# Performance work log

Hardware: AMD Instinct MI355X
Metric: run time of the kernel (lower is better)

The kernel has to match this reference:

```python
import jax, jax.numpy as jnp
import numpy as np

H = 1024      # hidden_size
NH = 16       # num_heads
HD = 128      # head_dim
ID = NH * HD  # inner_dim = 2048
EPS = 1e-6


def setup_inputs() -> dict:
    key = jax.random.key(0)
    ks = jax.random.split(key, 8)
    n = lambda k, shape, sc=1.0: jax.random.normal(k, shape, dtype=jnp.float32) * sc
    return {
        "x": n(ks[0], (1, H)),
        "rnn_state": n(ks[1], (1, NH, HD, HD)),
        "conv_state": n(ks[2], (1, 3 * ID, 3)),
        # learned parameters (nn.Linear stores W as [out_features, in_features])
        "W_qkv": n(ks[3], (3 * ID, H), 0.02),
        "W_z": n(ks[4], (ID, H), 0.02),
        "W_a": n(ks[5], (NH, H), 0.02),
        "norm_w": jnp.ones((HD,), jnp.float32),
        "W_out": n(ks[6], (H, ID), 0.02),
    }


def reference(x, rnn_state, conv_state, W_qkv, W_z, W_a, norm_w, W_out):
    # QKV projection: [1, 3*ID]
    qkv = x @ W_qkv.T
    q, k, v = jnp.split(qkv, 3, axis=-1)
    q = q.reshape(-1, NH, HD)
    k = k.reshape(-1, NH, HD)
    v = v.reshape(-1, NH, HD)

    # per-head scalar decay in (0,1): [1, NH, 1, 1]
    decay = jax.nn.sigmoid(x @ W_a.T)[:, :, None, None]

    # outer product k \otimes v: [1, NH, HD, HD]
    kv = k[..., :, None] * v[..., None, :]
    new_state = rnn_state * decay + kv

    # query readout: [1, NH, HD]
    y = jnp.einsum('bhd,bhde->bhe', q, new_state)

    # RMSNorm over head_dim
    y = y * jax.lax.rsqrt(jnp.mean(y * y, axis=-1, keepdims=True) + EPS) * norm_w
    y = y.reshape(-1, ID)

    # silu-gated combine and output projection
    z = x @ W_z.T
    y = y * (z * jax.nn.sigmoid(z))
    out = y @ W_out.T
    return (out, new_state, conv_state)
```

## Files before the change

### kernel.cpp

```cpp
#include <hip/hip_runtime.h>
#include <math.h>

#define H    1024
#define NH   16
#define HD   128
#define ID   2048
#define NROWS_A (3*ID + ID + NH)
#define MATVEC_BLOCKS (NROWS_A / 4)
#define CONV_FLOATS (3 * ID * 3)
#define CONV_BLOCKS (CONV_FLOATS / 4 / 256)
#define EPS 1e-6f

__device__ __forceinline__ float waveReduceSum(float v) {
#pragma unroll
    for (int off = 32; off > 0; off >>= 1) v += __shfl_down(v, off, 64);
    return v;
}
__device__ __forceinline__ float waveReduceSumAll(float v) {
#pragma unroll
    for (int off = 1; off < 64; off <<= 1) v += __shfl_xor(v, off, 64);
    return v;
}

__global__ __launch_bounds__(256) void matvec_qkvza(
    const float* __restrict__ x,
    const float* __restrict__ Wqkv,
    const float* __restrict__ Wz,
    const float* __restrict__ Wa,
    const float* __restrict__ conv,
    float* __restrict__ conv_out,
    float* __restrict__ out,
    float* __restrict__ ws_qkv,
    float* __restrict__ ws_zsig,
    float* __restrict__ ws_decay)
{
    if (blockIdx.x >= MATVEC_BLOCKS) {
        const int cb = blockIdx.x - MATVEC_BLOCKS;
        const int i = cb * 256 + threadIdx.x;
        ((float4*)conv_out)[i] = ((const float4*)conv)[i];
        if (cb == 0) {
            float4 z4 = {0.f, 0.f, 0.f, 0.f};
            ((float4*)out)[threadIdx.x] = z4;
        }
        return;
    }

    const int wave = threadIdx.x >> 6;
    const int lane = threadIdx.x & 63;
    const int r = blockIdx.x * 4 + wave;

    const float* row;
    if (r < 3 * ID)           row = Wqkv + (size_t)r * H;
    else if (r < 3 * ID + ID) row = Wz   + (size_t)(r - 3 * ID) * H;
    else                      row = Wa   + (size_t)(r - 3 * ID - ID) * H;

    const float4* row4 = (const float4*)row;
    const float4* x4   = (const float4*)x;

    float acc = 0.f;
#pragma unroll
    for (int t = 0; t < 4; ++t) {
        float4 w  = row4[lane + 64 * t];
        float4 xv = x4[lane + 64 * t];
        acc += w.x * xv.x + w.y * xv.y + w.z * xv.z + w.w * xv.w;
    }
    acc = waveReduceSum(acc);
    if (lane == 0) {
        if (r < 3 * ID) {
            ws_qkv[r] = acc;
        } else if (r < 3 * ID + ID) {
            const float sig = 1.f / (1.f + expf(-acc));
            ws_zsig[r - 3 * ID] = acc * sig;
        } else {
            ws_decay[r - 3 * ID - ID] = 1.f / (1.f + expf(-acc));
        }
    }
}

__global__ __launch_bounds__(1024) void state_gate_out(
    const float* __restrict__ state_in,
    const float* __restrict__ ws_qkv,
    const float* __restrict__ ws_decay,
    const float* __restrict__ ws_zsig,
    const float* __restrict__ normw,
    const float* __restrict__ Wout,
    float* __restrict__ state_out,
    float* __restrict__ out)
{
    const int h  = blockIdx.x >> 4;
    const int s  = blockIdx.x & 15;
    const int t  = threadIdx.x;
    const int c  = t & 31;
    const int dg = t >> 5;
    const int wv = t >> 6;
    const int lane = t & 63;

    __shared__ float4 part4[16][32];
    __shared__ float gated[HD];
    __shared__ float red2[2];

    const float decay = ws_decay[h];
    const float4 vv = ((const float4*)(ws_qkv + 2 * ID + h * HD))[c];
    const float4 q4 = ((const float4*)(ws_qkv + h * HD))[dg];
    const float4 k4 = ((const float4*)(ws_qkv + ID + h * HD))[dg];

    const float4* sin4 = (const float4*)(state_in  + (size_t)h * HD * HD);
    float4*       sout = (float4*)(state_out + (size_t)h * HD * HD);

    const bool do_write = (wv == s);

    float4 acc = {0.f, 0.f, 0.f, 0.f};
    const float qs[4] = {q4.x, q4.y, q4.z, q4.w};
    const float ks[4] = {k4.x, k4.y, k4.z, k4.w};
#pragma unroll
    for (int i = 0; i < 4; ++i) {
        const int d = dg * 4 + i;
        const float4 sv = sin4[d * 32 + c];
        float4 sn;
        sn.x = sv.x * decay + ks[i] * vv.x;
        sn.y = sv.y * decay + ks[i] * vv.y;
        sn.z = sv.z * decay + ks[i] * vv.z;
        sn.w = sv.w * decay + ks[i] * vv.w;
        if (do_write) sout[d * 32 + c] = sn;
        acc.x += qs[i] * sn.x;
        acc.y += qs[i] * sn.y;
        acc.z += qs[i] * sn.z;
        acc.w += qs[i] * sn.w;
    }
    acc.x += __shfl_xor(acc.x, 32, 64);
    acc.y += __shfl_xor(acc.y, 32, 64);
    acc.z += __shfl_xor(acc.z, 32, 64);
    acc.w += __shfl_xor(acc.w, 32, 64);
    if (lane < 32) part4[wv][c] = acc;
    __syncthreads();

    const float* partF = (const float*)part4;
    float y = 0.f;
    if (t < HD) {
#pragma unroll
        for (int w2 = 0; w2 < 16; ++w2) y += partF[w2 * HD + t];
        const float s2 = waveReduceSumAll(y * y);
        if (lane == 0) red2[t >> 6] = s2;
    }
    __syncthreads();
    if (t < HD) {
        const float scale = rsqrtf((red2[0] + red2[1]) * (1.f / HD) + EPS);
        gated[t] = y * scale * normw[t] * ws_zsig[h * HD + t];
    }
    __syncthreads();

    {
        const int rl = t >> 4;
        const int j  = t & 15;
        const int r  = s * 64 + rl;
        const float4* wrow = (const float4*)(Wout + (size_t)r * ID + h * HD);
        const float4* g4   = (const float4*)gated;
        const float4 w0 = wrow[j * 2],     w1 = wrow[j * 2 + 1];
        const float4 g0 = g4[j * 2],       g1 = g4[j * 2 + 1];
        float a = w0.x * g0.x + w0.y * g0.y + w0.z * g0.z + w0.w * g0.w
                + w1.x * g1.x + w1.y * g1.y + w1.z * g1.z + w1.w * g1.w;
        a += __shfl_xor(a, 1, 64);
        a += __shfl_xor(a, 2, 64);
        a += __shfl_xor(a, 4, 64);
        a += __shfl_xor(a, 8, 64);
        if (j == 0) atomicAdd(&out[r], a);
    }
}

extern "C" void kernel_launch(void* const* d_in, const int* in_sizes, int n_in,
                              void* d_out, int out_size, void* d_ws, size_t ws_size,
                              hipStream_t stream) {
    const float* x     = (const float*)d_in[0];
    const float* state = (const float*)d_in[1];
    const float* conv  = (const float*)d_in[2];
    const float* Wqkv  = (const float*)d_in[3];
    const float* Wz    = (const float*)d_in[4];
    const float* Wa    = (const float*)d_in[5];
    const float* normw = (const float*)d_in[6];
    const float* Wout  = (const float*)d_in[7];

    float* out       = (float*)d_out;
    float* new_state = out + H;
    float* conv_out  = new_state + (size_t)NH * HD * HD;

    float* ws       = (float*)d_ws;
    float* ws_qkv   = ws;
    float* ws_zsig  = ws + 6144;
    float* ws_decay = ws + 8192;

    matvec_qkvza<<<MATVEC_BLOCKS + CONV_BLOCKS, 256, 0, stream>>>(
        x, Wqkv, Wz, Wa, conv, conv_out, out, ws_qkv, ws_zsig, ws_decay);
    state_gate_out<<<NH * 16, 1024, 0, stream>>>(
        state, ws_qkv, ws_decay, ws_zsig, normw, Wout, new_state, out);
}
```

Before: 18.08 us.

## Process four rows per wave in matvec and prefetch Wout early

```diff
diff --git a/kernel.cpp b/kernel.cpp
--- a/kernel.cpp
+++ b/kernel.cpp
@@ -6,16 +6,12 @@
 #define HD   128
 #define ID   2048
 #define NROWS_A (3*ID + ID + NH)
-#define MATVEC_BLOCKS (NROWS_A / 4)
+#define NWAVES_A (NROWS_A / 4)
+#define MATVEC_BLOCKS (NWAVES_A / 4)
 #define CONV_FLOATS (3 * ID * 3)
 #define CONV_BLOCKS (CONV_FLOATS / 4 / 256)
 #define EPS 1e-6f
 
-__device__ __forceinline__ float waveReduceSum(float v) {
-#pragma unroll
-    for (int off = 32; off > 0; off >>= 1) v += __shfl_down(v, off, 64);
-    return v;
-}
 __device__ __forceinline__ float waveReduceSumAll(float v) {
 #pragma unroll
     for (int off = 1; off < 64; off <<= 1) v += __shfl_xor(v, off, 64);
@@ -47,32 +43,63 @@
 
     const int wave = threadIdx.x >> 6;
     const int lane = threadIdx.x & 63;
-    const int r = blockIdx.x * 4 + wave;
-
-    const float* row;
-    if (r < 3 * ID)           row = Wqkv + (size_t)r * H;
-    else if (r < 3 * ID + ID) row = Wz   + (size_t)(r - 3 * ID) * H;
-    else                      row = Wa   + (size_t)(r - 3 * ID - ID) * H;
-
-    const float4* row4 = (const float4*)row;
-    const float4* x4   = (const float4*)x;
-
-    float acc = 0.f;
-#pragma unroll
-    for (int t = 0; t < 4; ++t) {
-        float4 w  = row4[lane + 64 * t];
-        float4 xv = x4[lane + 64 * t];
-        acc += w.x * xv.x + w.y * xv.y + w.z * xv.z + w.w * xv.w;
-    }
-    acc = waveReduceSum(acc);
+    const int w  = blockIdx.x * 4 + wave;
+    const int r0 = w * 4;
+
+    const float* base;
+    int kind;
+    if (r0 < 3 * ID)      { base = Wqkv + (size_t)r0 * H;            kind = 0; }
+    else if (r0 < 4 * ID) { base = Wz + (size_t)(r0 - 3 * ID) * H;   kind = 1; }
+    else                  { base = Wa + (size_t)(r0 - 4 * ID) * H;   kind = 2; }
+
+    const float4* b4 = (const float4*)base;
+    const float4* x4 = (const float4*)x;
+
+    float4 xv[4];
+#pragma unroll
+    for (int i = 0; i < 4; ++i) xv[i] = x4[lane + 64 * i];
+
+    float4 wr[4][4];
+#pragma unroll
+    for (int rr = 0; rr < 4; ++rr)
+#pragma unroll
+        for (int i = 0; i < 4; ++i)
+            wr[rr][i] = b4[rr * 256 + lane + 64 * i];
+
+    float acc[4];
+#pragma unroll
+    for (int rr = 0; rr < 4; ++rr) {
+        float a = 0.f;
+#pragma unroll
+        for (int i = 0; i < 4; ++i)
+            a += wr[rr][i].x * xv[i].x + wr[rr][i].y * xv[i].y
+               + wr[rr][i].z * xv[i].z + wr[rr][i].w * xv[i].w;
+        acc[rr] = a;
+    }
+#pragma unroll
+    for (int off = 1; off < 64; off <<= 1) {
+#pragma unroll
+        for (int rr = 0; rr < 4; ++rr) acc[rr] += __shfl_xor(acc[rr], off, 64);
+    }
+
     if (lane == 0) {
-        if (r < 3 * ID) {
-            ws_qkv[r] = acc;
-        } else if (r < 3 * ID + ID) {
-            const float sig = 1.f / (1.f + expf(-acc));
-            ws_zsig[r - 3 * ID] = acc * sig;
+        if (kind == 0) {
+            float4 o = {acc[0], acc[1], acc[2], acc[3]};
+            *(float4*)(ws_qkv + r0) = o;
+        } else if (kind == 1) {
+            float4 o;
+            o.x = acc[0] / (1.f + expf(-acc[0]));
+            o.y = acc[1] / (1.f + expf(-acc[1]));
+            o.z = acc[2] / (1.f + expf(-acc[2]));
+            o.w = acc[3] / (1.f + expf(-acc[3]));
+            *(float4*)(ws_zsig + (r0 - 3 * ID)) = o;
         } else {
-            ws_decay[r - 3 * ID - ID] = 1.f / (1.f + expf(-acc));
+            float4 o;
+            o.x = 1.f / (1.f + expf(-acc[0]));
+            o.y = 1.f / (1.f + expf(-acc[1]));
+            o.z = 1.f / (1.f + expf(-acc[2]));
+            o.w = 1.f / (1.f + expf(-acc[3]));
+            *(float4*)(ws_decay + (r0 - 4 * ID)) = o;
         }
     }
 }
@@ -87,8 +114,8 @@
     float* __restrict__ state_out,
     float* __restrict__ out)
 {
-    const int h  = blockIdx.x >> 4;
-    const int s  = blockIdx.x & 15;
+    const int s  = blockIdx.x >> 4;
+    const int h  = blockIdx.x & 15;
     const int t  = threadIdx.x;
     const int c  = t & 31;
     const int dg = t >> 5;
@@ -98,6 +125,13 @@
     __shared__ float4 part4[16][32];
     __shared__ float gated[HD];
     __shared__ float red2[2];
+
+    const int rl = t >> 4;
+    const int j  = t & 15;
+    const int r  = s * 64 + rl;
+    const float4* wrow = (const float4*)(Wout + (size_t)r * ID + h * HD);
+    const float4 w0 = wrow[j * 2];
+    const float4 w1 = wrow[j * 2 + 1];
 
     const float decay = ws_decay[h];
     const float4 vv = ((const float4*)(ws_qkv + 2 * ID + h * HD))[c];
@@ -150,13 +184,8 @@
     __syncthreads();
 
     {
-        const int rl = t >> 4;
-        const int j  = t & 15;
-        const int r  = s * 64 + rl;
-        const float4* wrow = (const float4*)(Wout + (size_t)r * ID + h * HD);
-        const float4* g4   = (const float4*)gated;
-        const float4 w0 = wrow[j * 2],     w1 = wrow[j * 2 + 1];
-        const float4 g0 = g4[j * 2],       g1 = g4[j * 2 + 1];
+        const float4* g4 = (const float4*)gated;
+        const float4 g0 = g4[j * 2], g1 = g4[j * 2 + 1];
         float a = w0.x * g0.x + w0.y * g0.y + w0.z * g0.z + w0.w * g0.w
                 + w1.x * g1.x + w1.y * g1.y + w1.z * g1.z + w1.w * g1.w;
         a += __shfl_xor(a, 1, 64);
```

Result: slower. 20.95 us (+15.9%).
